# Performance work log

Hardware: AMD Instinct MI355X
Metric: run time of the kernel (lower is better)

Reference implementation:

```python
import jax, jax.numpy as jnp
import numpy as np

# ---- dims (see shape_source) ----
B, S, DH = 2, 2048, 2048
H, DN, DR, DV = 16, 128, 64, 128          # heads, nope, rope, v head dims
KV_LORA, Q_LORA = 512, 1024               # MLA latent ranks
HI, DI, TOPK = 8, 128, 1024               # indexer heads / dim / sparse top-k
BLK, FP8MAX, NEG = 128, 448.0, -1e30
ROPE_THETA = 10000.0
EPS = 1e-6


def _fp8_qdq_act(x):
    """DeepSeek block-128 fp8 activation quant-dequant (power-of-2 e8m0 scales)."""
    xb = x.reshape(x.shape[:-1] + (x.shape[-1] // BLK, BLK))
    amax = jnp.maximum(jnp.max(jnp.abs(xb), axis=-1, keepdims=True), 1e-4)
    scale = jnp.exp2(jnp.ceil(jnp.log2(amax / FP8MAX)))  # e8m0 = exact pow2
    q = jnp.clip(xb / scale, -FP8MAX, FP8MAX).astype(jnp.float8_e4m3fn).astype(jnp.float32)
    return (q * scale).reshape(x.shape)


def _fp8_qdq_weight(w):
    """128x128 block fp8 weight quant-dequant (mirrors _dequant_fp8_weight)."""
    o, i = w.shape
    po, pi = (-o) % BLK, (-i) % BLK
    wp = jnp.pad(w, ((0, po), (0, pi)))
    wb = wp.reshape((o + po) // BLK, BLK, (i + pi) // BLK, BLK)
    amax = jnp.maximum(jnp.max(jnp.abs(wb), axis=(1, 3), keepdims=True), 1e-4)
    scale = amax / FP8MAX
    q = jnp.clip(wb / scale, -FP8MAX, FP8MAX).astype(jnp.float8_e4m3fn).astype(jnp.float32)
    return (q * scale).reshape(o + po, i + pi)[:o, :i]


def _fp8_linear(x, w):
    return _fp8_qdq_act(x) @ _fp8_qdq_weight(w).T


def _rms(x, w):
    return x * jax.lax.rsqrt(jnp.mean(x * x, axis=-1, keepdims=True) + EPS) * w


def _rope_cos_sin(positions):
    inv = 1.0 / (ROPE_THETA ** (jnp.arange(0, DR, 2, dtype=jnp.float32) / DR))
    ang = positions.astype(jnp.float32)[..., None] * inv  # [B,S,DR/2]
    return jnp.cos(ang), jnp.sin(ang)


def _apply_rope(x, cos, sin):
    x1, x2 = jnp.split(x, 2, axis=-1)
    return jnp.concatenate([x1 * cos - x2 * sin, x2 * cos + x1 * sin], axis=-1)


def _forward(hidden, Wqa, q_norm_w, Wqb, Wkva, kv_norm_w, Wkvb, Wiq, Wik, Wig, Wo, positions):
    # --- MLA query path: fp8 down-proj -> RMSNorm -> fp8 up-proj ---
    q_a = _rms(_fp8_linear(hidden, Wqa), q_norm_w)                 # [B,S,Q_LORA]
    q = _fp8_linear(q_a, Wqb).reshape(B, S, H, DN + DR)
    q_nope, q_rope = q[..., :DN], q[..., DN:]
    # --- MLA compressed KV latent ---
    kv_a = _fp8_linear(hidden, Wkva)                               # [B,S,KV_LORA+DR]
    c_kv, k_rope = kv_a[..., :KV_LORA], kv_a[..., KV_LORA:]
    c_kv = _rms(c_kv, kv_norm_w)
    kv = _fp8_linear(c_kv, Wkvb).reshape(B, S, H, DN + DV)
    k_nope, v = kv[..., :DN], kv[..., DN:]
    # --- RoPE on the decoupled rope dims ---
    cos, sin = _rope_cos_sin(positions)                            # [B,S,DR/2]
    q_rope = _apply_rope(q_rope, cos[:, :, None, :], sin[:, :, None, :])
    k_rope = _apply_rope(k_rope, cos, sin)                         # shared across heads
    # --- Indexer: lightweight scores -> causal top-k KV selection ---
    qi = (hidden @ Wiq.T).reshape(B, S, HI, DI)
    ki = hidden @ Wik.T                                            # [B,S,DI]
    wgt = (hidden @ Wig.T) * (HI ** -0.5)                          # [B,S,HI]
    sc = jax.nn.relu(jnp.einsum('bqhd,bkd->bhqk', qi, ki))
    isc = jnp.einsum('bqh,bhqk->bqk', wgt, sc)                     # [B,S,S]
    tri = jnp.tril(jnp.ones((S, S), dtype=bool))
    isc = jnp.where(tri[None], isc, NEG)
    _, topi = jax.lax.top_k(isc, TOPK)                             # [B,S,TOPK]
    sel = jnp.zeros((B, S, S), dtype=bool).at[
        jnp.arange(B)[:, None, None], jnp.arange(S)[None, :, None], topi].set(True)
    mask = sel & tri[None]                                         # sparse+causal
    # --- sparse MLA attention over selected KV ---
    q_full = jnp.concatenate([q_nope, q_rope], axis=-1)            # [B,S,H,DN+DR]
    k_full = jnp.concatenate(
        [k_nope, jnp.broadcast_to(k_rope[:, :, None, :], (B, S, H, DR))], axis=-1)
    logits = jnp.einsum('bqhd,bkhd->bhqk', q_full, k_full) * ((DN + DR) ** -0.5)
    logits = jnp.where(mask[:, None], logits, NEG)
    p = jax.nn.softmax(logits, axis=-1)
    ctx = jnp.einsum('bhqk,bkhd->bqhd', p, v).reshape(B, S, H * DV)
    return _fp8_linear(ctx, Wo)                                    # [B,S,DH]


def setup_inputs() -> dict:
    key = jax.random.key(0)
    ks = jax.random.split(key, 12)
    def w(k, o, i):
        return jax.random.normal(k, (o, i), dtype=jnp.float32) * (i ** -0.5)
    return {
        'hidden': jax.random.normal(ks[0], (B, S, DH), dtype=jnp.float32),
        'Wqa': w(ks[1], Q_LORA, DH),
        'q_norm_w': jnp.ones((Q_LORA,), dtype=jnp.float32),
        'Wqb': w(ks[2], H * (DN + DR), Q_LORA),
        'Wkva': w(ks[3], KV_LORA + DR, DH),
        'kv_norm_w': jnp.ones((KV_LORA,), dtype=jnp.float32),
        'Wkvb': w(ks[4], H * (DN + DV), KV_LORA),
        'Wiq': w(ks[5], HI * DI, DH),
        'Wik': w(ks[6], DI, DH),
        'Wig': w(ks[7], HI, DH),
        'Wo': w(ks[8], DH, H * DV),
        'positions': jnp.broadcast_to(jnp.arange(S, dtype=jnp.int32), (B, S)),
    }


def reference(hidden, Wqa, q_norm_w, Wqb, Wkva, kv_norm_w, Wkvb, Wiq, Wik, Wig, Wo, positions):
    return _forward(hidden, Wqa, q_norm_w, Wqb, Wkva, kv_norm_w, Wkvb, Wiq, Wik, Wig, Wo, positions)
```

## Files before the change

kernel.cpp:

```cpp
#include <hip/hip_runtime.h>
#include <math.h>

namespace {
constexpr int kB = 2, kS = 2048, kDH = 2048, kH = 16, kDN = 128, kDR = 64, kDV = 128;
constexpr int kKvLora = 512, kQLora = 1024, kHI = 8, kDI = 128, kTopK = 1024;
constexpr int kNTok = kB * kS;
constexpr float kNeg = -1e30f;

constexpr size_t OFF_SC    = 0;
constexpr size_t OFF_SEL_B = 4096;
constexpr size_t OFF_WGT_B = OFF_SEL_B + 1048576;
constexpr size_t OFF_KRH_B = OFF_WGT_B + 131072;
constexpr size_t OFF_KRL_B = OFF_KRH_B + 524288;
constexpr size_t OFF_WOB_B = OFF_KRL_B + 524288;
constexpr size_t POOL      = OFF_WOB_B + 8388608;
constexpr size_t B_HIDQ = POOL;
constexpr size_t B_WQA  = POOL + 16777216;
constexpr size_t B_WQB  = POOL + 20971520;
constexpr size_t B_WKVA = POOL + 27262976;
constexpr size_t B_WKVB = POOL + 29884416;
constexpr size_t B_QAF  = POOL + 34078720;
constexpr size_t B_QAB  = POOL + 50855936;
constexpr size_t B_KVA  = POOL + 59244544;
constexpr size_t B_CKV  = POOL + 68681728;
constexpr size_t B_QH   = POOL + 72876032;
constexpr size_t B_QL   = POOL + 98041856;
constexpr size_t B_KNH  = POOL + 123207680;
constexpr size_t B_KNL  = POOL + 139984896;
constexpr size_t B_VTH  = POOL;
constexpr size_t B_VTL  = POOL + 34078720;
constexpr size_t B_CTXB = POOL + 50855936;
constexpr size_t A_HHI  = POOL + 16777216;
constexpr size_t A_HLO  = POOL + 33554432;
constexpr size_t A_WQKH = POOL + 50331648;
constexpr size_t A_WQKL = POOL + 55050240;
constexpr size_t A_QIKH = POOL + 59768832;
constexpr size_t A_QIKL = POOL + 69206016;
constexpr size_t A_ISC  = POOL + 78643200;
constexpr size_t WS_NEED = POOL + 156762112;
}

typedef __attribute__((ext_vector_type(4))) float f32x4;
typedef __attribute__((ext_vector_type(8))) short bf16x8;
typedef __attribute__((address_space(1))) const void gvoid;
typedef __attribute__((address_space(3))) void lvoid;

__device__ __forceinline__ float fp8_e4m3_qdq(float x) {
  float ax = fabsf(x);
  int e;
  (void)frexpf(ax, &e);
  int ee = e - 1;
  if (ee < -6) ee = -6;
  float q = ldexpf(1.0f, ee - 3);
  float y = rintf(ax / q) * q;
  return (x < 0.0f) ? -y : y;
}

__device__ __forceinline__ float act_scale_from_amax(float amax) {
  float t = amax / 448.0f;
  unsigned u = __float_as_uint(t);
  int e = (int)((u >> 23) & 255u) - 127;
  if (u & 0x7fffffu) e += 1;
  return __uint_as_float((unsigned)(e + 127) << 23);
}

__device__ __forceinline__ float clamp448(float v) {
  return fminf(fmaxf(v, -448.0f), 448.0f);
}

__device__ __forceinline__ unsigned short f32_to_bf16(float f) {
  unsigned u = __float_as_uint(f);
  unsigned r = (u + 0x7FFFu + ((u >> 16) & 1u)) >> 16;
  return (unsigned short)r;
}
__device__ __forceinline__ float bf16_to_f32(unsigned short h) {
  return __uint_as_float((unsigned)h << 16);
}

__global__ __launch_bounds__(256) void fill_kernel(float* p, int n, float v) {
  int i = blockIdx.x * 256 + threadIdx.x;
  if (i < n) p[i] = v;
}

__global__ __launch_bounds__(256) void hidden_prep_kernel(const float* __restrict__ X,
                                                          unsigned short* __restrict__ HI,
                                                          unsigned short* __restrict__ LO,
                                                          unsigned short* __restrict__ QB) {
  int wid = blockIdx.x * 4 + (threadIdx.x >> 6);
  int lane = threadIdx.x & 63;
  const float* x = X + (size_t)wid * 128;
  float v0 = x[lane], v1 = x[lane + 64];
  size_t o0 = (size_t)wid * 128 + lane, o1 = o0 + 64;
  unsigned short h0 = f32_to_bf16(v0);
  HI[o0] = h0; LO[o0] = f32_to_bf16(v0 - bf16_to_f32(h0));
  unsigned short h1 = f32_to_bf16(v1);
  HI[o1] = h1; LO[o1] = f32_to_bf16(v1 - bf16_to_f32(h1));
  float am = fmaxf(fabsf(v0), fabsf(v1));
#pragma unroll
  for (int m = 32; m >= 1; m >>= 1) am = fmaxf(am, __shfl_xor(am, m, 64));
  am = fmaxf(am, 1e-4f);
  float s = act_scale_from_amax(am);
  QB[o0] = f32_to_bf16(fp8_e4m3_qdq(clamp448(v0 / s)) * s);
  QB[o1] = f32_to_bf16(fp8_e4m3_qdq(clamp448(v1 / s)) * s);
}

__global__ __launch_bounds__(256) void fused_weight5_kernel(const float* __restrict__ W0,
                                                            const float* __restrict__ W1,
                                                            const float* __restrict__ W2,
                                                            const float* __restrict__ W3,
                                                            const float* __restrict__ W4,
                                                            float* __restrict__ SCB,
                                                            unsigned short* __restrict__ B0,
                                                            unsigned short* __restrict__ B1,
                                                            unsigned short* __restrict__ B2,
                                                            unsigned short* __restrict__ B3,
                                                            unsigned short* __restrict__ B4) {
  int bid = blockIdx.x;
  const float* W; unsigned short* WB; float* SC; int O, I, KBX, loc;
  if (bid < 128)      { W = W0; WB = B0; SC = SCB + 0;   O = 1024; I = 2048; KBX = 16; loc = bid; }
  else if (bid < 320) { W = W1; WB = B1; SC = SCB + 128; O = 3072; I = 1024; KBX = 8;  loc = bid - 128; }
  else if (bid < 400) { W = W2; WB = B2; SC = SCB + 320; O = 576;  I = 2048; KBX = 16; loc = bid - 320; }
  else if (bid < 528) { W = W3; WB = B3; SC = SCB + 400; O = 4096; I = 512;  KBX = 4;  loc = bid - 400; }
  else                { W = W4; WB = B4; SC = SCB + 528; O = 2048; I = 2048; KBX = 16; loc = bid - 528; }
  int kb = loc % KBX, ob = loc / KBX;
  int bo = ob * 128, bi = kb * 128;
  int tid = threadIdx.x;
  __shared__ float red[256];
  __shared__ float s_scale;
  float am = 0.0f;
  for (int idx = tid; idx < 128 * 128; idx += 256) {
    int r = bo + (idx >> 7), c = bi + (idx & 127);
    if (r < O) am = fmaxf(am, fabsf(W[(size_t)r * I + c]));
  }
  red[tid] = am; __syncthreads();
  for (int s = 128; s >= 1; s >>= 1) {
    if (tid < s) red[tid] = fmaxf(red[tid], red[tid + s]);
    __syncthreads();
  }
  if (tid == 0) {
    float sc = fmaxf(red[0], 1e-4f) / 448.0f;
    SC[(size_t)ob * KBX + kb] = sc;
    s_scale = sc;
  }
  __syncthreads();
  float sc = s_scale;
  for (int idx = tid; idx < 128 * 128; idx += 256) {
    int r = bo + (idx >> 7), c = bi + (idx & 127);
    unsigned short v = 0;
    if (r < O) v = f32_to_bf16(fp8_e4m3_qdq(clamp448(W[(size_t)r * I + c] / sc)));
    WB[(size_t)r * I + c] = v;
  }
}

__global__ __launch_bounds__(256) void split_bf16x2_kernel(const float* __restrict__ X,
                                                           unsigned short* __restrict__ HI,
                                                           unsigned short* __restrict__ LO,
                                                           size_t n) {
  size_t i = (size_t)blockIdx.x * 256 + threadIdx.x;
  if (i >= n) return;
  float x = X[i];
  unsigned short h = f32_to_bf16(x);
  HI[i] = h;
  LO[i] = f32_to_bf16(x - bf16_to_f32(h));
}

__global__ __launch_bounds__(256) void rms_qdq_kernel(const float* __restrict__ X,
                                                      const float* __restrict__ G,
                                                      unsigned short* __restrict__ Y,
                                                      int C, int xs, int ys) {
  int row = blockIdx.x, tid = threadIdx.x;
  __shared__ float xr[1024];
  __shared__ float red[256];
  const float* x = X + (size_t)row * xs;
  float ssq = 0.0f;
  for (int i = tid; i < C; i += 256) { float v = x[i]; xr[i] = v; ssq += v * v; }
  red[tid] = ssq; __syncthreads();
  for (int s = 128; s >= 1; s >>= 1) { if (tid < s) red[tid] += red[tid + s]; __syncthreads(); }
  float inv = 1.0f / sqrtf(red[0] / (float)C + 1e-6f);
  __syncthreads();
  int wv = tid >> 6, lane = tid & 63;
  for (int blk = wv; blk < C / 128; blk += 4) {
    int i0 = blk * 128 + lane, i1 = i0 + 64;
    float y0 = xr[i0] * inv * G[i0];
    float y1 = xr[i1] * inv * G[i1];
    float am = fmaxf(fabsf(y0), fabsf(y1));
#pragma unroll
    for (int m = 32; m >= 1; m >>= 1) am = fmaxf(am, __shfl_xor(am, m, 64));
    am = fmaxf(am, 1e-4f);
    float s = act_scale_from_amax(am);
    Y[(size_t)row * ys + i0] = f32_to_bf16(fp8_e4m3_qdq(clamp448(y0 / s)) * s);
    Y[(size_t)row * ys + i1] = f32_to_bf16(fp8_e4m3_qdq(clamp448(y1 / s)) * s);
  }
}

template <int OMODE, bool SCALED>
__global__ __launch_bounds__(256) void mfma_gemm_kernel(const unsigned short* __restrict__ A,
                                                        const unsigned short* __restrict__ B,
                                                        const float* __restrict__ Bsc,
                                                        float* __restrict__ C,
                                                        unsigned short* __restrict__ O1,
                                                        unsigned short* __restrict__ O2,
                                                        unsigned short* __restrict__ O3,
                                                        unsigned short* __restrict__ O4,
                                                        int N, int K, int ldc) {
  __shared__ unsigned short lA[128 * 64];
  __shared__ unsigned short lB[128 * 64];
  const int tid = threadIdx.x;
  const int wave = tid >> 6, lane = tid & 63;
  const int wr = (wave >> 1) * 64, wc = (wave & 1) * 64;
  const int m0 = blockIdx.y * 128, n0 = blockIdx.x * 128;
  const int KB = K >> 7;
  const int frow = lane & 15, fk = (lane >> 4) * 8;

  f32x4 mainAcc[4][4];
  f32x4 part[4][4];
  const f32x4 vzero = {0.f, 0.f, 0.f, 0.f};
#pragma unroll
  for (int i = 0; i < 4; ++i)
#pragma unroll
    for (int j = 0; j < 4; ++j) { mainAcc[i][j] = vzero; part[i][j] = vzero; }

  const int nkt = K >> 6;
  for (int kt = 0; kt < nkt; ++kt) {
    const int k0 = kt << 6;
    __syncthreads();
#pragma unroll
    for (int it = 0; it < 4; ++it) {
      int o = it * 4096 + wave * 1024 + lane * 16;
      int row = o >> 7;
      int kb = o & 127;
      const char* ga = (const char*)(A + (size_t)(m0 + row) * K + k0) + kb;
      const char* gb = (const char*)(B + (size_t)(n0 + row) * K + k0) + kb;
      __builtin_amdgcn_global_load_lds((gvoid*)ga, (lvoid*)((char*)lA + o), 16, 0, 0);
      __builtin_amdgcn_global_load_lds((gvoid*)gb, (lvoid*)((char*)lB + o), 16, 0, 0);
    }
    __syncthreads();
#pragma unroll
    for (int ks = 0; ks < 2; ++ks) {
      bf16x8 af[4], bfr[4];
#pragma unroll
      for (int i = 0; i < 4; ++i)
        af[i] = *(const bf16x8*)&lA[(wr + i * 16 + frow) * 64 + ks * 32 + fk];
#pragma unroll
      for (int j = 0; j < 4; ++j)
        bfr[j] = *(const bf16x8*)&lB[(wc + j * 16 + frow) * 64 + ks * 32 + fk];
#pragma unroll
      for (int i = 0; i < 4; ++i)
#pragma unroll
        for (int j = 0; j < 4; ++j)
          part[i][j] = __builtin_amdgcn_mfma_f32_16x16x32_bf16(af[i], bfr[j], part[i][j], 0, 0, 0);
    }
    if (SCALED) {
      float bs = Bsc[(size_t)(n0 >> 7) * KB + (k0 >> 7)];
#pragma unroll
      for (int i = 0; i < 4; ++i)
#pragma unroll
        for (int j = 0; j < 4; ++j) {
          mainAcc[i][j] += part[i][j] * bs;
          part[i][j] = vzero;
        }
    }
  }
  const int crow0 = (lane >> 4) * 4;
  const int ccol = lane & 15;
#pragma unroll
  for (int i = 0; i < 4; ++i) {
#pragma unroll
    for (int j = 0; j < 4; ++j) {
      f32x4 v = SCALED ? mainAcc[i][j] : part[i][j];
      int col = n0 + wc + j * 16 + ccol;
      if (col < N) {
#pragma unroll
        for (int r = 0; r < 4; ++r) {
          int m = m0 + wr + i * 16 + crow0 + r;
          float val = v[r];
          if (OMODE == 0) {
            C[(size_t)m * ldc + col] = val;
          } else if (OMODE == 1) {
            int hh = col / 192, d = col - hh * 192;
            int bb = m >> 11, s = m & 2047;
            size_t off = ((size_t)((bb * 16 + hh) * 2048 + s)) * 192 + d;
            unsigned short hi = f32_to_bf16(val);
            O1[off] = hi;
            O2[off] = f32_to_bf16(val - bf16_to_f32(hi));
          } else {
            int hh = col >> 8, d = col & 255;
            int bb = m >> 11, s = m & 2047;
            if (d < 128) {
              size_t off = ((size_t)((bb * 16 + hh) * 2048 + s)) * 128 + d;
              unsigned short hi = f32_to_bf16(val);
              O1[off] = hi;
              O2[off] = f32_to_bf16(val - bf16_to_f32(hi));
            } else {
              size_t off = ((size_t)((bb * 16 + hh) * 128 + (d - 128))) * 2048 + s;
              unsigned short hi = f32_to_bf16(val);
              O3[off] = hi;
              O4[off] = f32_to_bf16(val - bf16_to_f32(hi));
            }
          }
        }
      }
    }
  }
}

__global__ __launch_bounds__(256) void mfma_gemm3_kernel(const unsigned short* __restrict__ Ah,
                                                         const unsigned short* __restrict__ Al,
                                                         const unsigned short* __restrict__ Bh,
                                                         const unsigned short* __restrict__ Bl,
                                                         unsigned short* __restrict__ OH,
                                                         unsigned short* __restrict__ OL,
                                                         int K, int ldc) {
  if (blockIdx.x < 8 && !(blockIdx.y & 8)) return;
  __shared__ unsigned short lAh[128 * 64], lAl[128 * 64];
  __shared__ unsigned short lBh[128 * 64], lBl[128 * 64];
  const int tid = threadIdx.x;
  const int wave = tid >> 6, lane = tid & 63;
  const int wr = (wave >> 1) * 64, wc = (wave & 1) * 64;
  const int m0 = blockIdx.y * 128, n0 = blockIdx.x * 128;
  const int frow = lane & 15, fk = (lane >> 4) * 8;

  f32x4 part[4][4];
  const f32x4 vzero = {0.f, 0.f, 0.f, 0.f};
#pragma unroll
  for (int i = 0; i < 4; ++i)
#pragma unroll
    for (int j = 0; j < 4; ++j) part[i][j] = vzero;

  const int nkt = K >> 6;
  for (int kt = 0; kt < nkt; ++kt) {
    const int k0 = kt << 6;
    __syncthreads();
#pragma unroll
    for (int it = 0; it < 4; ++it) {
      int o = it * 4096 + wave * 1024 + lane * 16;
      int row = o >> 7;
      int kb = o & 127;
      size_t ga = (size_t)(m0 + row) * K + k0;
      size_t gb = (size_t)(n0 + row) * K + k0;
      __builtin_amdgcn_global_load_lds((gvoid*)((const char*)(Ah + ga) + kb), (lvoid*)((char*)lAh + o), 16, 0, 0);
      __builtin_amdgcn_global_load_lds((gvoid*)((const char*)(Al + ga) + kb), (lvoid*)((char*)lAl + o), 16, 0, 0);
      __builtin_amdgcn_global_load_lds((gvoid*)((const char*)(Bh + gb) + kb), (lvoid*)((char*)lBh + o), 16, 0, 0);
      __builtin_amdgcn_global_load_lds((gvoid*)((const char*)(Bl + gb) + kb), (lvoid*)((char*)lBl + o), 16, 0, 0);
    }
    __syncthreads();
#pragma unroll
    for (int ks = 0; ks < 2; ++ks) {
      bf16x8 ah[4], al[4], bh[4], bl[4];
#pragma unroll
      for (int i = 0; i < 4; ++i) {
        ah[i] = *(const bf16x8*)&lAh[(wr + i * 16 + frow) * 64 + ks * 32 + fk];
        al[i] = *(const bf16x8*)&lAl[(wr + i * 16 + frow) * 64 + ks * 32 + fk];
      }
#pragma unroll
      for (int j = 0; j < 4; ++j) {
        bh[j] = *(const bf16x8*)&lBh[(wc + j * 16 + frow) * 64 + ks * 32 + fk];
        bl[j] = *(const bf16x8*)&lBl[(wc + j * 16 + frow) * 64 + ks * 32 + fk];
      }
#pragma unroll
      for (int i = 0; i < 4; ++i)
#pragma unroll
        for (int j = 0; j < 4; ++j) {
          part[i][j] = __builtin_amdgcn_mfma_f32_16x16x32_bf16(ah[i], bh[j], part[i][j], 0, 0, 0);
          part[i][j] = __builtin_amdgcn_mfma_f32_16x16x32_bf16(ah[i], bl[j], part[i][j], 0, 0, 0);
          part[i][j] = __builtin_amdgcn_mfma_f32_16x16x32_bf16(al[i], bh[j], part[i][j], 0, 0, 0);
        }
    }
  }
  const int crow0 = (lane >> 4) * 4;
  const int ccol = lane & 15;
#pragma unroll
  for (int i = 0; i < 4; ++i)
#pragma unroll
    for (int j = 0; j < 4; ++j) {
      int col = n0 + wc + j * 16 + ccol;
#pragma unroll
      for (int r = 0; r < 4; ++r) {
        float val = part[i][j][r];
        size_t off = (size_t)(m0 + wr + i * 16 + crow0 + r) * ldc + col;
        unsigned short hi = f32_to_bf16(val);
        OH[off] = hi;
        OL[off] = f32_to_bf16(val - bf16_to_f32(hi));
      }
    }
}

__global__ __launch_bounds__(256) void gemm_f32_kernel(const float* __restrict__ A,
                                                       const float* __restrict__ Bw,
                                                       float* __restrict__ C,
                                                       int N, int K, float alpha, int rowskip) {
  if (rowskip && !(blockIdx.y & rowskip)) return;
  __shared__ __align__(16) float As[16][68];
  __shared__ __align__(16) float Bs[16][68];
  int n0 = blockIdx.x * 64;
  int m0 = blockIdx.y * 64;
  int tid = threadIdx.x;
  int tx = tid & 15, ty = tid >> 4;
  float acc[4][4] = {};
  for (int k0 = 0; k0 < K; k0 += 16) {
#pragma unroll
    for (int t = 0; t < 4; ++t) {
      int idx = tid + t * 256;
      int rr = idx >> 4;
      int kk = idx & 15;
      As[kk][rr] = A[(size_t)(m0 + rr) * K + (k0 + kk)];
      Bs[kk][rr] = (n0 + rr < N) ? Bw[(size_t)(n0 + rr) * K + (k0 + kk)] : 0.0f;
    }
    __syncthreads();
#pragma unroll
    for (int kk = 0; kk < 16; ++kk) {
      float4 a = *(const float4*)&As[kk][ty * 4];
      float4 b = *(const float4*)&Bs[kk][tx * 4];
      float av[4] = {a.x, a.y, a.z, a.w};
      float bv[4] = {b.x, b.y, b.z, b.w};
#pragma unroll
      for (int i = 0; i < 4; ++i)
#pragma unroll
        for (int j = 0; j < 4; ++j) acc[i][j] += av[i] * bv[j];
    }
    __syncthreads();
  }
#pragma unroll
  for (int i = 0; i < 4; ++i) {
    int m = m0 + ty * 4 + i;
#pragma unroll
    for (int j = 0; j < 4; ++j) {
      int n = n0 + tx * 4 + j;
      if (n < N) C[(size_t)m * N + n] = alpha * acc[i][j];
    }
  }
}

__global__ __launch_bounds__(64) void rope_split_kernel(unsigned short* __restrict__ Qh,
                                                        unsigned short* __restrict__ Ql,
                                                        const float* __restrict__ KVA,
                                                        unsigned short* __restrict__ Krh,
                                                        unsigned short* __restrict__ Krl,
                                                        const int* __restrict__ POS) {
  int t = blockIdx.x;
  int tid = threadIdx.x;
  int b = t >> 11, s = t & 2047;
  __shared__ float cs[32], sn[32];
  if (tid < 32) {
    int pos = POS[t];
    double inv = pow(10000.0, -((double)(2 * tid) / 64.0));
    float ang = (float)pos * (float)inv;
    cs[tid] = cosf(ang);
    sn[tid] = sinf(ang);
  }
  __syncthreads();
  if (tid < 32) {
    const float* kr = KVA + (size_t)t * (kKvLora + kDR) + kKvLora;
    float x1 = kr[tid], x2 = kr[32 + tid];
    float y1 = x1 * cs[tid] - x2 * sn[tid];
    float y2 = x2 * cs[tid] + x1 * sn[tid];
    unsigned short h1 = f32_to_bf16(y1);
    Krh[(size_t)t * 64 + tid] = h1;
    Krl[(size_t)t * 64 + tid] = f32_to_bf16(y1 - bf16_to_f32(h1));
    unsigned short h2 = f32_to_bf16(y2);
    Krh[(size_t)t * 64 + 32 + tid] = h2;
    Krl[(size_t)t * 64 + 32 + tid] = f32_to_bf16(y2 - bf16_to_f32(h2));
  }
  for (int it = tid; it < kH * 32; it += 64) {
    int h = it >> 5, i = it & 31;
    size_t base = ((size_t)((b * 16 + h) * 2048 + s)) * 192 + 128;
    float x1 = bf16_to_f32(Qh[base + i]) + bf16_to_f32(Ql[base + i]);
    float x2 = bf16_to_f32(Qh[base + 32 + i]) + bf16_to_f32(Ql[base + 32 + i]);
    float y1 = x1 * cs[i] - x2 * sn[i];
    float y2 = x2 * cs[i] + x1 * sn[i];
    unsigned short h1 = f32_to_bf16(y1);
    Qh[base + i] = h1;
    Ql[base + i] = f32_to_bf16(y1 - bf16_to_f32(h1));
    unsigned short h2 = f32_to_bf16(y2);
    Qh[base + 32 + i] = h2;
    Ql[base + 32 + i] = f32_to_bf16(y2 - bf16_to_f32(h2));
  }
}

__global__ __launch_bounds__(256) void isc_mfma_kernel(const unsigned short* __restrict__ QIKH,
                                                       const unsigned short* __restrict__ QIKL,
                                                       const float* __restrict__ WGT,
                                                       float* __restrict__ ISC) {
  const int qt = blockIdx.y + 16;
  const int kt = blockIdx.x;
  if (kt > qt) return;
  const int b = blockIdx.z;
  const int q0 = qt * 64, k0 = kt * 64;
  const int tid = threadIdx.x, wave = tid >> 6, lane = tid & 63;
  const int fr = lane & 15, fg = lane >> 4;

  __shared__ unsigned short KiH[4 * 64 * 40], KiL[4 * 64 * 40];
  __shared__ float wgs[64 * 8];

  {
    int key = tid >> 2, sub = (tid & 3) * 8;
    size_t rb = (size_t)(b * kS + k0 + key) * 1152 + 1024;
#pragma unroll
    for (int kc = 0; kc < 4; ++kc) {
      *(bf16x8*)&KiH[kc * 2560 + key * 40 + sub] = *(const bf16x8*)&QIKH[rb + kc * 32 + sub];
      *(bf16x8*)&KiL[kc * 2560 + key * 40 + sub] = *(const bf16x8*)&QIKL[rb + kc * 32 + sub];
    }
#pragma unroll
    for (int t = 0; t < 2; ++t) {
      int i = t * 256 + tid;
      wgs[i] = WGT[(size_t)(b * kS + q0 + (i >> 3)) * kHI + (i & 7)];
    }
  }
  const size_t qrow = (size_t)(b * kS + q0 + wave * 16 + fr) * 1152;
  f32x4 sacc[4];
  const f32x4 vzero = {0.f, 0.f, 0.f, 0.f};
#pragma unroll
  for (int j = 0; j < 4; ++j) sacc[j] = vzero;

  bf16x8 qAh[4], qAl[4], qBh[4], qBl[4];
#define LOADQ(DH_, DL_, H_)                                                     \
  _Pragma("unroll") for (int kc = 0; kc < 4; ++kc) {                            \
    DH_[kc] = *(const bf16x8*)&QIKH[qrow + (H_)*128 + kc * 32 + fg * 8];        \
    DL_[kc] = *(const bf16x8*)&QIKL[qrow + (H_)*128 + kc * 32 + fg * 8];        \
  }
  LOADQ(qAh, qAl, 0)
  __syncthreads();
#define MFMA_HEAD(QH_, QL_, H_)                                                 \
  {                                                                             \
    f32x4 acc[4];                                                               \
    _Pragma("unroll") for (int j = 0; j < 4; ++j) acc[j] = vzero;               \
    _Pragma("unroll") for (int kc = 0; kc < 4; ++kc) {                          \
      _Pragma("unroll") for (int j = 0; j < 4; ++j) {                           \
        bf16x8 kh = *(const bf16x8*)&KiH[kc * 2560 + (j * 16 + fr) * 40 + fg * 8]; \
        bf16x8 kl = *(const bf16x8*)&KiL[kc * 2560 + (j * 16 + fr) * 40 + fg * 8]; \
        acc[j] = __builtin_amdgcn_mfma_f32_16x16x32_bf16(QH_[kc], kh, acc[j], 0, 0, 0); \
        acc[j] = __builtin_amdgcn_mfma_f32_16x16x32_bf16(QH_[kc], kl, acc[j], 0, 0, 0); \
        acc[j] = __builtin_amdgcn_mfma_f32_16x16x32_bf16(QL_[kc], kh, acc[j], 0, 0, 0); \
      }                                                                         \
    }                                                                           \
    float wv[4];                                                                \
    _Pragma("unroll") for (int r = 0; r < 4; ++r)                               \
        wv[r] = wgs[(wave * 16 + fg * 4 + r) * 8 + (H_)];                       \
    _Pragma("unroll") for (int j = 0; j < 4; ++j)                               \
      _Pragma("unroll") for (int r = 0; r < 4; ++r)                             \
        sacc[j][r] += fmaxf(acc[j][r], 0.0f) * wv[r];                           \
  }
#pragma unroll
  for (int hp = 0; hp < 4; ++hp) {
    int h0 = hp * 2;
    LOADQ(qBh, qBl, h0 + 1)
    MFMA_HEAD(qAh, qAl, h0)
    if (hp < 3) LOADQ(qAh, qAl, h0 + 2)
    MFMA_HEAD(qBh, qBl, h0 + 1)
  }
#undef LOADQ
#undef MFMA_HEAD
#pragma unroll
  for (int r = 0; r < 4; ++r) {
    size_t ob = (size_t)(b * kS + q0 + wave * 16 + fg * 4 + r) * kS + k0;
#pragma unroll
    for (int j = 0; j < 4; ++j) ISC[ob + j * 16 + fr] = sacc[j][r];
  }
}

__global__ __launch_bounds__(256) void topk_kernel(const float* __restrict__ ISC,
                                                   unsigned* __restrict__ SEL) {
  int row = blockIdx.x;
  int q = row & (kS - 1);
  int L = q + 1;
  unsigned* selrow = SEL + (size_t)row * (kS / 32);
  int tid = threadIdx.x;
  if (L <= kTopK) {
    if (tid < kS / 32) {
      int base = tid * 32;
      unsigned w;
      if (base + 32 <= L) w = 0xFFFFFFFFu;
      else if (base >= L) w = 0u;
      else w = (1u << (L - base)) - 1u;
      selrow[tid] = w;
    }
    return;
  }
  __shared__ unsigned keys[kS];
  __shared__ unsigned hist[256];
  __shared__ unsigned sfx[256];
  __shared__ unsigned msk[kS / 32];
  __shared__ unsigned pick[2];
  if (tid < kS / 32) msk[tid] = 0u;
  const float* x = ISC + (size_t)row * kS;
  for (int k = tid; k < L; k += 256) {
    unsigned u = __float_as_uint(x[k]);
    keys[k] = (u & 0x80000000u) ? ~u : (u | 0x80000000u);
  }
  __syncthreads();
  unsigned prefix = 0u;
  int r = kTopK;
  for (int shift = 24; shift >= 0; shift -= 8) {
    hist[tid] = 0u;
    __syncthreads();
    unsigned hm = (shift == 24) ? 0u : (0xFFFFFFFFu << (shift + 8));
    for (int k = tid; k < L; k += 256) {
      unsigned key = keys[k];
      if ((key & hm) == (prefix & hm)) atomicAdd(&hist[(key >> shift) & 255u], 1u);
    }
    __syncthreads();
    sfx[tid] = hist[tid];
    __syncthreads();
#pragma unroll
    for (int step = 1; step < 256; step <<= 1) {
      unsigned add = (tid + step < 256) ? sfx[tid + step] : 0u;
      __syncthreads();
      sfx[tid] += add;
      __syncthreads();
    }
    {
      unsigned Tb = sfx[tid];
      unsigned Tb1 = (tid < 255) ? sfx[tid + 1] : 0u;
      if (Tb1 < (unsigned)r && (unsigned)r <= Tb) {
        pick[0] = (unsigned)tid;
        pick[1] = (unsigned)r - Tb1;
      }
    }
    __syncthreads();
    prefix |= pick[0] << shift;
    r = (int)pick[1];
    __syncthreads();
  }
  unsigned T = prefix;
  int ties_take = r;
  int base = tid * 8;
  int cnt = 0;
#pragma unroll
  for (int j = 0; j < 8; ++j) {
    int k = base + j;
    if (k < L && keys[k] == T) ++cnt;
  }
  hist[tid] = (unsigned)cnt;
  __syncthreads();
  sfx[tid] = hist[tid];
  __syncthreads();
#pragma unroll
  for (int step = 1; step < 256; step <<= 1) {
    unsigned add = (tid >= step) ? sfx[tid - step] : 0u;
    __syncthreads();
    sfx[tid] += add;
    __syncthreads();
  }
  int trank = (tid == 0) ? 0 : (int)sfx[tid - 1];
  unsigned bits = 0u;
#pragma unroll
  for (int j = 0; j < 8; ++j) {
    int k = base + j;
    if (k < L) {
      unsigned key = keys[k];
      bool s;
      if (key > T) s = true;
      else if (key == T) { s = trank < ties_take; ++trank; }
      else s = false;
      if (s) bits |= (1u << j);
    }
  }
  atomicOr(&msk[tid >> 2], bits << ((tid & 3) * 8));
  __syncthreads();
  if (tid < kS / 32) selrow[tid] = msk[tid];
}

__global__ __launch_bounds__(256) void attn_mfma_kernel(const unsigned short* __restrict__ Qh,
                                                        const unsigned short* __restrict__ Ql,
                                                        const unsigned short* __restrict__ Knh,
                                                        const unsigned short* __restrict__ Knl,
                                                        const unsigned short* __restrict__ Krh,
                                                        const unsigned short* __restrict__ Krl,
                                                        const unsigned short* __restrict__ Vth,
                                                        const unsigned short* __restrict__ Vtl,
                                                        const unsigned* __restrict__ SEL,
                                                        unsigned short* __restrict__ CTXB) {
  const int flat = blockIdx.x;
  const int qt = 31 - (flat >> 4);
  const int h = flat & 15;
  const int b = blockIdx.y;
  const int q0 = qt * 64;
  const int tid = threadIdx.x, wave = tid >> 6, lane = tid & 63;
  const int fr = lane & 15, fg = lane >> 4;
  const float scale = 0.07216878364870323f;

  __shared__ unsigned short KsH[2 * 64 * 40], KsL[2 * 64 * 40];
  __shared__ unsigned short Vs[128 * 72];
  __shared__ unsigned selw[64][2];
  unsigned short* Ph = KsH;
  unsigned short* Pl = KsL;

  bf16x8 qh[6], ql[6];
  {
    const size_t qbase = ((size_t)((b * 16 + h) * 2048 + q0 + wave * 16 + fr)) * 192;
#pragma unroll
    for (int kc = 0; kc < 6; ++kc) {
      qh[kc] = *(const bf16x8*)&Qh[qbase + kc * 32 + fg * 8];
      ql[kc] = *(const bf16x8*)&Ql[qbase + kc * 32 + fg * 8];
    }
  }
  float m_run[4], l_run[4];
#pragma unroll
  for (int r = 0; r < 4; ++r) { m_run[r] = kNeg; l_run[r] = 0.0f; }
  f32x4 O[8];
  const f32x4 vzero = {0.f, 0.f, 0.f, 0.f};
#pragma unroll
  for (int j = 0; j < 8; ++j) O[j] = vzero;

  const int key = tid >> 2, sub = (tid & 3) * 8;
  const size_t knbase = (size_t)((b * 16 + h) * 2048) * 128;
  const size_t krbase = (size_t)(b * 2048) * 64;
  const size_t vbase0 = ((size_t)((b * 16 + h) * 128)) * 2048;

  const int nkt = qt + 1;
  for (int kt = 0; kt < nkt; ++kt) {
    const int k0 = kt * 64;
    const size_t vbase = vbase0 + k0;
    unsigned selreg = 0;
    if (tid < 128)
      selreg = SEL[(size_t)(b * kS + q0 + (tid >> 1)) * (kS / 32) + (k0 >> 5) + (tid & 1)];
    bf16x8 kh_pre[2], kl_pre[2];
    {
      size_t src = knbase + (size_t)(k0 + key) * 128 + sub;
      kh_pre[0] = *(const bf16x8*)&Knh[src];
      kl_pre[0] = *(const bf16x8*)&Knl[src];
    }
    bf16x8 vpre[4];
#pragma unroll
    for (int it = 0; it < 4; ++it) {
      int idx = it * 256 + tid;
      int dv = idx >> 3, ks8 = (idx & 7) * 8;
      vpre[it] = *(const bf16x8*)&Vth[vbase + (size_t)dv * 2048 + ks8];
    }
    __syncthreads();
    if (tid < 128) selw[tid >> 1][tid & 1] = selreg;
    f32x4 acc[4];
#pragma unroll
    for (int j = 0; j < 4; ++j) acc[j] = vzero;
#pragma unroll
    for (int kc = 0; kc < 6; ++kc) {
      const int buf = (kc & 1) * 2560;
      *(bf16x8*)&KsH[buf + key * 40 + sub] = kh_pre[kc & 1];
      *(bf16x8*)&KsL[buf + key * 40 + sub] = kl_pre[kc & 1];
      if (kc < 5) {
        if (kc + 1 < 4) {
          size_t src = knbase + (size_t)(k0 + key) * 128 + (kc + 1) * 32 + sub;
          kh_pre[(kc + 1) & 1] = *(const bf16x8*)&Knh[src];
          kl_pre[(kc + 1) & 1] = *(const bf16x8*)&Knl[src];
        } else {
          size_t src = krbase + (size_t)(k0 + key) * 64 + (kc - 3) * 32 + sub;
          kh_pre[(kc + 1) & 1] = *(const bf16x8*)&Krh[src];
          kl_pre[(kc + 1) & 1] = *(const bf16x8*)&Krl[src];
        }
      }
      __syncthreads();
#pragma unroll
      for (int j = 0; j < 4; ++j) {
        bf16x8 kh = *(const bf16x8*)&KsH[buf + (j * 16 + fr) * 40 + fg * 8];
        bf16x8 kl = *(const bf16x8*)&KsL[buf + (j * 16 + fr) * 40 + fg * 8];
        acc[j] = __builtin_amdgcn_mfma_f32_16x16x32_bf16(qh[kc], kh, acc[j], 0, 0, 0);
        acc[j] = __builtin_amdgcn_mfma_f32_16x16x32_bf16(qh[kc], kl, acc[j], 0, 0, 0);
        acc[j] = __builtin_amdgcn_mfma_f32_16x16x32_bf16(ql[kc], kh, acc[j], 0, 0, 0);
      }
    }
    float p[4][4];
    float fsc[4];
#pragma unroll
    for (int r = 0; r < 4; ++r) {
      int row = wave * 16 + fg * 4 + r;
      float sv[4];
      float vmax = kNeg;
#pragma unroll
      for (int j = 0; j < 4; ++j) {
        int col = j * 16 + fr;
        bool bit = (selw[row][col >> 5] >> (col & 31)) & 1u;
        float s = bit ? acc[j][r] * scale : kNeg;
        sv[j] = s;
        vmax = fmaxf(vmax, s);
      }
#pragma unroll
      for (int m = 1; m <= 8; m <<= 1) vmax = fmaxf(vmax, __shfl_xor(vmax, m, 64));
      float newm = fmaxf(m_run[r], vmax);
      float sum = 0.0f;
#pragma unroll
      for (int j = 0; j < 4; ++j) {
        float pp = (sv[j] < -1e29f) ? 0.0f : __expf(sv[j] - newm);
        p[j][r] = pp;
        sum += pp;
      }
#pragma unroll
      for (int m = 1; m <= 8; m <<= 1) sum += __shfl_xor(sum, m, 64);
      fsc[r] = __expf(m_run[r] - newm);
      l_run[r] = l_run[r] * fsc[r] + sum;
      m_run[r] = newm;
    }
#pragma unroll
    for (int j = 0; j < 8; ++j)
#pragma unroll
      for (int r = 0; r < 4; ++r) O[j][r] *= fsc[r];
    __syncthreads();
#pragma unroll
    for (int r = 0; r < 4; ++r) {
      int row = wave * 16 + fg * 4 + r;
#pragma unroll
      for (int j = 0; j < 4; ++j) {
        int col = j * 16 + fr;
        float pp = p[j][r];
        unsigned short hi = f32_to_bf16(pp);
        Ph[row * 72 + col] = hi;
        Pl[row * 72 + col] = f32_to_bf16(pp - bf16_to_f32(hi));
      }
    }
#pragma unroll
    for (int it = 0; it < 4; ++it) {
      int idx = it * 256 + tid;
      int dv = idx >> 3, ks8 = (idx & 7) * 8;
      *(bf16x8*)&Vs[dv * 72 + ks8] = vpre[it];
    }
#pragma unroll
    for (int it = 0; it < 4; ++it) {
      int idx = it * 256 + tid;
      int dv = idx >> 3, ks8 = (idx & 7) * 8;
      vpre[it] = *(const bf16x8*)&Vtl[vbase + (size_t)dv * 2048 + ks8];
    }
    __syncthreads();
#pragma unroll
    for (int kk = 0; kk < 2; ++kk) {
      bf16x8 pah = *(const bf16x8*)&Ph[(wave * 16 + fr) * 72 + kk * 32 + fg * 8];
      bf16x8 pal = *(const bf16x8*)&Pl[(wave * 16 + fr) * 72 + kk * 32 + fg * 8];
#pragma unroll
      for (int j = 0; j < 8; ++j) {
        bf16x8 vb = *(const bf16x8*)&Vs[(j * 16 + fr) * 72 + kk * 32 + fg * 8];
        O[j] = __builtin_amdgcn_mfma_f32_16x16x32_bf16(pah, vb, O[j], 0, 0, 0);
        O[j] = __builtin_amdgcn_mfma_f32_16x16x32_bf16(pal, vb, O[j], 0, 0, 0);
      }
    }
    __syncthreads();
#pragma unroll
    for (int it = 0; it < 4; ++it) {
      int idx = it * 256 + tid;
      int dv = idx >> 3, ks8 = (idx & 7) * 8;
      *(bf16x8*)&Vs[dv * 72 + ks8] = vpre[it];
    }
    __syncthreads();
#pragma unroll
    for (int kk = 0; kk < 2; ++kk) {
      bf16x8 pah = *(const bf16x8*)&Ph[(wave * 16 + fr) * 72 + kk * 32 + fg * 8];
#pragma unroll
      for (int j = 0; j < 8; ++j) {
        bf16x8 vb = *(const bf16x8*)&Vs[(j * 16 + fr) * 72 + kk * 32 + fg * 8];
        O[j] = __builtin_amdgcn_mfma_f32_16x16x32_bf16(pah, vb, O[j], 0, 0, 0);
      }
    }
  }
#pragma unroll
  for (int r = 0; r < 4; ++r) {
    float inv = 1.0f / l_run[r];
    float vals[8];
    float am = 0.0f;
#pragma unroll
    for (int j = 0; j < 8; ++j) {
      vals[j] = O[j][r] * inv;
      am = fmaxf(am, fabsf(vals[j]));
    }
#pragma unroll
    for (int m = 1; m <= 8; m <<= 1) am = fmaxf(am, __shfl_xor(am, m, 64));
    am = fmaxf(am, 1e-4f);
    float s = act_scale_from_amax(am);
    size_t obase = (size_t)(b * kS + q0 + wave * 16 + fg * 4 + r) * 2048 + h * 128;
#pragma unroll
    for (int j = 0; j < 8; ++j)
      CTXB[obase + j * 16 + fr] = f32_to_bf16(fp8_e4m3_qdq(clamp448(vals[j] / s)) * s);
  }
}

extern "C" void kernel_launch(void* const* d_in, const int* in_sizes, int n_in,
                              void* d_out, int out_size, void* d_ws, size_t ws_size,
                              hipStream_t stream) {
  (void)in_sizes; (void)n_in;

  const float* hidden = (const float*)d_in[0];
  const float* Wqa    = (const float*)d_in[1];
  const float* qnw    = (const float*)d_in[2];
  const float* Wqb    = (const float*)d_in[3];
  const float* Wkva   = (const float*)d_in[4];
  const float* kvnw   = (const float*)d_in[5];
  const float* Wkvb   = (const float*)d_in[6];
  const float* Wiq    = (const float*)d_in[7];
  const float* Wik    = (const float*)d_in[8];
  const float* Wig    = (const float*)d_in[9];
  const float* Wo     = (const float*)d_in[10];
  const int*   pos    = (const int*)d_in[11];
  char* ws = (char*)d_ws;
  float* out = (float*)d_out;

  if (ws_size < WS_NEED) {
    fill_kernel<<<dim3((out_size + 255) / 256), dim3(256), 0, stream>>>(out, out_size, 54321.0f);
    return;
  }

  float* scbase = (float*)(ws + OFF_SC);
  float* scWqa  = scbase + 0;
  float* scWqb  = scbase + 128;
  float* scWkva = scbase + 320;
  float* scWkvb = scbase + 400;
  float* scWo   = scbase + 528;
  unsigned* sel = (unsigned*)(ws + OFF_SEL_B);
  float* wgt    = (float*)(ws + OFF_WGT_B);
  unsigned short* krh = (unsigned short*)(ws + OFF_KRH_B);
  unsigned short* krl = (unsigned short*)(ws + OFF_KRL_B);
  unsigned short* wo_b = (unsigned short*)(ws + OFF_WOB_B);

  unsigned short* h_hi  = (unsigned short*)(ws + A_HHI);
  unsigned short* h_lo  = (unsigned short*)(ws + A_HLO);
  unsigned short* wqk_h = (unsigned short*)(ws + A_WQKH);
  unsigned short* wqk_l = (unsigned short*)(ws + A_WQKL);
  unsigned short* qik_h = (unsigned short*)(ws + A_QIKH);
  unsigned short* qik_l = (unsigned short*)(ws + A_QIKL);
  float* isc = (float*)(ws + A_ISC);

  unsigned short* hidq_b = (unsigned short*)(ws + B_HIDQ);
  unsigned short* wqa_b  = (unsigned short*)(ws + B_WQA);
  unsigned short* wqb_b  = (unsigned short*)(ws + B_WQB);
  unsigned short* wkva_b = (unsigned short*)(ws + B_WKVA);
  unsigned short* wkvb_b = (unsigned short*)(ws + B_WKVB);
  float* qa_f   = (float*)(ws + B_QAF);
  unsigned short* qa_b  = (unsigned short*)(ws + B_QAB);
  float* kva    = (float*)(ws + B_KVA);
  unsigned short* ckv_b = (unsigned short*)(ws + B_CKV);
  unsigned short* q_h   = (unsigned short*)(ws + B_QH);
  unsigned short* q_l   = (unsigned short*)(ws + B_QL);
  unsigned short* kn_h  = (unsigned short*)(ws + B_KNH);
  unsigned short* kn_l  = (unsigned short*)(ws + B_KNL);
  unsigned short* v_th  = (unsigned short*)(ws + B_VTH);
  unsigned short* v_tl  = (unsigned short*)(ws + B_VTL);
  unsigned short* ctx_b = (unsigned short*)(ws + B_CTXB);

  hidden_prep_kernel<<<dim3(16384), dim3(256), 0, stream>>>(hidden, h_hi, h_lo, hidq_b);
  split_bf16x2_kernel<<<dim3(8192),  dim3(256), 0, stream>>>(Wiq, wqk_h, wqk_l, (size_t)kHI * kDI * kDH);
  split_bf16x2_kernel<<<dim3(1024),  dim3(256), 0, stream>>>(Wik, wqk_h + (size_t)1024 * kDH, wqk_l + (size_t)1024 * kDH, (size_t)kDI * kDH);
  gemm_f32_kernel<<<dim3(1, 64), dim3(256), 0, stream>>>(hidden, Wig, wgt, kHI, kDH, 0.35355339059327373f, 16);
  mfma_gemm3_kernel<<<dim3(9, 32), dim3(256), 0, stream>>>(h_hi, h_lo, wqk_h, wqk_l, qik_h, qik_l, kDH, 1152);
  isc_mfma_kernel<<<dim3(32, 16, kB), dim3(256), 0, stream>>>(qik_h, qik_l, wgt, isc);
  topk_kernel<<<dim3(kNTok), dim3(256), 0, stream>>>(isc, sel);

  fused_weight5_kernel<<<dim3(784), dim3(256), 0, stream>>>(Wqa, Wqb, Wkva, Wkvb, Wo, scbase,
                                                            wqa_b, wqb_b, wkva_b, wkvb_b, wo_b);

  mfma_gemm_kernel<0, true><<<dim3(8, 32), dim3(256), 0, stream>>>(hidq_b, wqa_b, scWqa, qa_f, nullptr, nullptr, nullptr, nullptr, 1024, kDH, 1024);
  rms_qdq_kernel<<<dim3(kNTok), dim3(256), 0, stream>>>(qa_f, qnw, qa_b, kQLora, kQLora, kQLora);
  mfma_gemm_kernel<1, true><<<dim3(24, 32), dim3(256), 0, stream>>>(qa_b, wqb_b, scWqb, nullptr, q_h, q_l, nullptr, nullptr, 3072, kQLora, 3072);
  mfma_gemm_kernel<0, true><<<dim3(5, 32), dim3(256), 0, stream>>>(hidq_b, wkva_b, scWkva, kva, nullptr, nullptr, nullptr, nullptr, 576, kDH, 576);
  rms_qdq_kernel<<<dim3(kNTok), dim3(256), 0, stream>>>(kva, kvnw, ckv_b, kKvLora, kKvLora + kDR, kKvLora);
  rope_split_kernel<<<dim3(kNTok), dim3(64), 0, stream>>>(q_h, q_l, kva, krh, krl, pos);
  mfma_gemm_kernel<2, true><<<dim3(32, 32), dim3(256), 0, stream>>>(ckv_b, wkvb_b, scWkvb, nullptr, kn_h, kn_l, v_th, v_tl, 4096, kKvLora, 4096);

  attn_mfma_kernel<<<dim3(512, kB), dim3(256), 0, stream>>>(q_h, q_l, kn_h, kn_l, krh, krl, v_th, v_tl, sel, ctx_b);
  mfma_gemm_kernel<0, true><<<dim3(16, 32), dim3(256), 0, stream>>>(ctx_b, wo_b, scWo, out, nullptr, nullptr, nullptr, nullptr, kDH, kH * kDV, 2048);
}
```

Before: 950.2 us.

## Split longest causal attention query tiles across two blocks with combine kernel

The longest 8 query tiles (qt 24..31) are each split into two key-range halves handled by separate blocks, which write unnormalized partial O, running max and sum to workspace. A new combine kernel merges the halves with the log-sum-exp rescale and then does the fp8 quant-dequant to bf16. The schedule is reordered so that split work interleaves with mid-length tiles. The goal is to balance the causal triangle's load tail across CUs, at the cost of an extra launch and partial-buffer traffic.

```diff
diff --git a/kernel.cpp b/kernel.cpp
--- a/kernel.cpp
+++ b/kernel.cpp
@@ -30,6 +30,8 @@
 constexpr size_t B_VTH  = POOL;
 constexpr size_t B_VTL  = POOL + 34078720;
 constexpr size_t B_CTXB = POOL + 50855936;
+constexpr size_t B_OPART = POOL + 16777216;
+constexpr size_t B_MPART = POOL + 33554432;
 constexpr size_t A_HHI  = POOL + 16777216;
 constexpr size_t A_HLO  = POOL + 33554432;
 constexpr size_t A_WQKH = POOL + 50331648;
@@ -669,11 +671,19 @@
                                                         const unsigned short* __restrict__ Vth,
                                                         const unsigned short* __restrict__ Vtl,
                                                         const unsigned* __restrict__ SEL,
+                                                        float* __restrict__ OPART,
+                                                        float* __restrict__ MPART,
                                                         unsigned short* __restrict__ CTXB) {
   const int flat = blockIdx.x;
-  const int qt = 31 - (flat >> 4);
+  const int j2 = flat >> 4;
   const int h = flat & 15;
   const int b = blockIdx.y;
+  int qt, kt0, kt1, half;
+  if (j2 < 8)       { qt = 23 - j2; kt0 = 0; kt1 = qt + 1; half = -1; }
+  else if (j2 < 24) { int idx = j2 - 8; qt = 31 - (idx >> 1); half = idx & 1;
+                      int nt = qt + 1, mid = nt >> 1;
+                      kt0 = half ? mid : 0; kt1 = half ? nt : mid; }
+  else              { qt = 39 - j2; kt0 = 0; kt1 = qt + 1; half = -1; }
   const int q0 = qt * 64;
   const int tid = threadIdx.x, wave = tid >> 6, lane = tid & 63;
   const int fr = lane & 15, fg = lane >> 4;
@@ -707,8 +717,7 @@
   const size_t krbase = (size_t)(b * 2048) * 64;
   const size_t vbase0 = ((size_t)((b * 16 + h) * 128)) * 2048;
 
-  const int nkt = qt + 1;
-  for (int kt = 0; kt < nkt; ++kt) {
+  for (int kt = kt0; kt < kt1; ++kt) {
     const int k0 = kt * 64;
     const size_t vbase = vbase0 + k0;
     unsigned selreg = 0;
@@ -848,25 +857,73 @@
       }
     }
   }
-#pragma unroll
-  for (int r = 0; r < 4; ++r) {
-    float inv = 1.0f / l_run[r];
-    float vals[8];
-    float am = 0.0f;
-#pragma unroll
-    for (int j = 0; j < 8; ++j) {
-      vals[j] = O[j][r] * inv;
-      am = fmaxf(am, fabsf(vals[j]));
-    }
-#pragma unroll
-    for (int m = 1; m <= 8; m <<= 1) am = fmaxf(am, __shfl_xor(am, m, 64));
-    am = fmaxf(am, 1e-4f);
-    float s = act_scale_from_amax(am);
-    size_t obase = (size_t)(b * kS + q0 + wave * 16 + fg * 4 + r) * 2048 + h * 128;
-#pragma unroll
-    for (int j = 0; j < 8; ++j)
-      CTXB[obase + j * 16 + fr] = f32_to_bf16(fp8_e4m3_qdq(clamp448(vals[j] / s)) * s);
-  }
+  if (half < 0) {
+#pragma unroll
+    for (int r = 0; r < 4; ++r) {
+      float inv = 1.0f / l_run[r];
+      float vals[8];
+      float am = 0.0f;
+#pragma unroll
+      for (int j = 0; j < 8; ++j) {
+        vals[j] = O[j][r] * inv;
+        am = fmaxf(am, fabsf(vals[j]));
+      }
+#pragma unroll
+      for (int m = 1; m <= 8; m <<= 1) am = fmaxf(am, __shfl_xor(am, m, 64));
+      am = fmaxf(am, 1e-4f);
+      float s = act_scale_from_amax(am);
+      size_t obase = (size_t)(b * kS + q0 + wave * 16 + fg * 4 + r) * 2048 + h * 128;
+#pragma unroll
+      for (int j = 0; j < 8; ++j)
+        CTXB[obase + j * 16 + fr] = f32_to_bf16(fp8_e4m3_qdq(clamp448(vals[j] / s)) * s);
+    }
+  } else {
+    const int p_idx = ((b * 16 + h) * 8 + (qt - 24)) * 2 + half;
+    float* Ob = OPART + (size_t)p_idx * 8192;
+    float* Mb = MPART + p_idx * 128;
+#pragma unroll
+    for (int r = 0; r < 4; ++r) {
+      int row = wave * 16 + fg * 4 + r;
+#pragma unroll
+      for (int j = 0; j < 8; ++j) Ob[row * 128 + j * 16 + fr] = O[j][r];
+      if (fr == 0) { Mb[row] = m_run[r]; Mb[64 + row] = l_run[r]; }
+    }
+  }
+}
+
+__global__ __launch_bounds__(256) void attn_combine_kernel(const float* __restrict__ OPART,
+                                                           const float* __restrict__ MPART,
+                                                           unsigned short* __restrict__ CTXB) {
+  const int bx = blockIdx.x;
+  const int b = blockIdx.y;
+  const int qtl = bx >> 4, h = bx & 15;
+  const int qt = 24 + qtl;
+  const int tid = threadIdx.x;
+  const int row = tid >> 2, cg = tid & 3;
+  const int p0 = ((b * 16 + h) * 8 + qtl) * 2;
+  float m1 = MPART[p0 * 128 + row],       l1 = MPART[p0 * 128 + 64 + row];
+  float m2 = MPART[(p0 + 1) * 128 + row], l2 = MPART[(p0 + 1) * 128 + 64 + row];
+  float m = fmaxf(m1, m2);
+  float f1 = __expf(m1 - m), f2 = __expf(m2 - m);
+  float inv = 1.0f / (l1 * f1 + l2 * f2);
+  const float* O1 = OPART + (size_t)p0 * 8192 + row * 128 + cg * 32;
+  const float* O2 = OPART + (size_t)(p0 + 1) * 8192 + row * 128 + cg * 32;
+  float vals[32];
+  float am = 0.0f;
+#pragma unroll
+  for (int i = 0; i < 32; ++i) {
+    float v = (O1[i] * f1 + O2[i] * f2) * inv;
+    vals[i] = v;
+    am = fmaxf(am, fabsf(v));
+  }
+  am = fmaxf(am, __shfl_xor(am, 1, 64));
+  am = fmaxf(am, __shfl_xor(am, 2, 64));
+  am = fmaxf(am, 1e-4f);
+  float s = act_scale_from_amax(am);
+  size_t obase = (size_t)(b * kS + qt * 64 + row) * 2048 + h * 128 + cg * 32;
+#pragma unroll
+  for (int i = 0; i < 32; ++i)
+    CTXB[obase + i] = f32_to_bf16(fp8_e4m3_qdq(clamp448(vals[i] / s)) * s);
 }
 
 extern "C" void kernel_launch(void* const* d_in, const int* in_sizes, int n_in,
@@ -930,6 +987,8 @@
   unsigned short* v_th  = (unsigned short*)(ws + B_VTH);
   unsigned short* v_tl  = (unsigned short*)(ws + B_VTL);
   unsigned short* ctx_b = (unsigned short*)(ws + B_CTXB);
+  float* opart = (float*)(ws + B_OPART);
+  float* mpart = (float*)(ws + B_MPART);
 
   hidden_prep_kernel<<<dim3(16384), dim3(256), 0, stream>>>(hidden, h_hi, h_lo, hidq_b);
   split_bf16x2_kernel<<<dim3(8192),  dim3(256), 0, stream>>>(Wiq, wqk_h, wqk_l, (size_t)kHI * kDI * kDH);
@@ -950,6 +1009,7 @@
   rope_split_kernel<<<dim3(kNTok), dim3(64), 0, stream>>>(q_h, q_l, kva, krh, krl, pos);
   mfma_gemm_kernel<2, true><<<dim3(32, 32), dim3(256), 0, stream>>>(ckv_b, wkvb_b, scWkvb, nullptr, kn_h, kn_l, v_th, v_tl, 4096, kKvLora, 4096);
 
-  attn_mfma_kernel<<<dim3(512, kB), dim3(256), 0, stream>>>(q_h, q_l, kn_h, kn_l, krh, krl, v_th, v_tl, sel, ctx_b);
+  attn_mfma_kernel<<<dim3(640, kB), dim3(256), 0, stream>>>(q_h, q_l, kn_h, kn_l, krh, krl, v_th, v_tl, sel, opart, mpart, ctx_b);
+  attn_combine_kernel<<<dim3(128, kB), dim3(256), 0, stream>>>(opart, mpart, ctx_b);
   mfma_gemm_kernel<0, true><<<dim3(16, 32), dim3(256), 0, stream>>>(ctx_b, wo_b, scWo, out, nullptr, nullptr, nullptr, nullptr, kDH, kH * kDV, 2048);
 }
```

Measured after the change: 960.9 us. About the same (+1.1%).
